# Kernel tuning notes

Measured on AMD Instinct MI355X. Metric: run time of the kernel, lower is better.

The kernel has to match this reference:

```python
import jax, jax.numpy as jnp
import numpy as np

N_NODES = 100000
N_EDGES = 1600000
IN_CH = 64
HID = 64
OUT_CH = 64
N_LAYERS = 4
LN_EPS = 1e-5
GEN_EPS = 1e-7


def setup_inputs() -> dict:
    key = jax.random.key(0)
    ks = jax.random.split(key, 16)
    s = 0.05
    return {
        "x": jax.random.normal(ks[0], (N_NODES, IN_CH), jnp.float32),
        "edge_attr": jax.random.normal(ks[1], (N_EDGES, IN_CH), jnp.float32),
        "edge_index": jax.random.randint(ks[2], (2, N_EDGES), 0, N_NODES, jnp.int32),
        "W_ne": jax.random.normal(ks[3], (IN_CH, HID), jnp.float32) * s,
        "b_ne": jnp.zeros((HID,), jnp.float32),
        "W_ee": jax.random.normal(ks[4], (IN_CH, HID), jnp.float32) * s,
        "b_ee": jnp.zeros((HID,), jnp.float32),
        "W_conv": jax.random.normal(ks[5], (N_LAYERS, HID, HID), jnp.float32) * s,
        "b_conv": jnp.zeros((N_LAYERS, HID), jnp.float32),
        "t": jnp.ones((N_LAYERS,), jnp.float32),
        "gamma": jnp.ones((N_LAYERS, HID), jnp.float32),
        "beta": jnp.zeros((N_LAYERS, HID), jnp.float32),
        "W_lin": jax.random.normal(ks[6], (HID, OUT_CH), jnp.float32) * s,
        "b_lin": jnp.zeros((OUT_CH,), jnp.float32),
    }


def _layer_norm(x, g, b):
    mu = jnp.mean(x, axis=-1, keepdims=True)
    var = jnp.mean(jnp.square(x - mu), axis=-1, keepdims=True)
    return (x - mu) * jax.lax.rsqrt(var + LN_EPS) * g + b


def _gen_conv(h, e, src, dst, W, b, t):
    # GENConv: msg = relu(x_j + edge_attr) + eps; per-dst channel-wise softmax
    # with temperature t; mlp (single Linear) applied to (aggr + x).
    msg = jnp.maximum(h[src] + e, 0.0) + GEN_EPS        # [E, D]
    w = msg * t
    m = jax.ops.segment_max(w, dst, num_segments=N_NODES)  # [N, D]
    ex = jnp.exp(w - m[dst])
    denom = jax.ops.segment_sum(ex, dst, num_segments=N_NODES)
    alpha = ex / (denom[dst] + 1e-16)
    aggr = jax.ops.segment_sum(alpha * msg, dst, num_segments=N_NODES)
    return (aggr + h) @ W + b


def reference(x, edge_attr, edge_index, W_ne, b_ne, W_ee, b_ee,
              W_conv, b_conv, t, gamma, beta, W_lin, b_lin):
    src, dst = edge_index[0], edge_index[1]
    h = x @ W_ne + b_ne              # node_encoder
    e = edge_attr @ W_ee + b_ee      # edge_encoder
    # layers[0].conv applied directly
    h = _gen_conv(h, e, src, dst, W_conv[0], b_conv[0], t[0])
    # remaining layers: pre-norm -> relu -> (dropout=identity, eval) -> conv + residual
    for i in range(1, N_LAYERS):
        z = jnp.maximum(_layer_norm(h, gamma[i], beta[i]), 0.0)
        h = _gen_conv(z, e, src, dst, W_conv[i], b_conv[i], t[i]) + h
    z = jnp.maximum(_layer_norm(h, gamma[0], beta[0]), 0.0)
    return z @ W_lin + b_lin
```

## Files before the change

### kernel.cpp

```cpp
#include <hip/hip_runtime.h>
#include <math.h>

#define NN 100000
#define NE 1600000
#define NB ((NN + 255) / 256)

typedef short bf16x8 __attribute__((ext_vector_type(8)));
typedef unsigned short u16x8 __attribute__((ext_vector_type(8)));
typedef float f32x4 __attribute__((ext_vector_type(4)));
typedef unsigned int u32x4 __attribute__((ext_vector_type(4)));

#define EQ_SCALE 0.025196850393700787f
#define EQ_INV   39.6875f

__device__ __forceinline__ short f2bf(float f) {
    union { float f; unsigned u; } x; x.f = f;
    unsigned r = x.u + 0x7fffu + ((x.u >> 16) & 1u);
    return (short)(r >> 16);
}
__device__ __forceinline__ float bf2f(unsigned short s) {
    union { unsigned u; float f; } x; x.u = ((unsigned)s) << 16;
    return x.f;
}
__device__ __forceinline__ signed char f2q8(float f) {
    float q = rintf(f * EQ_INV);
    q = fminf(127.f, fmaxf(-127.f, q));
    return (signed char)(int)q;
}
__device__ __forceinline__ float q82f(signed char c) {
    return (float)(int)c * EQ_SCALE;
}

__global__ void hist_kernel(const int* __restrict__ dst, int* __restrict__ deg) {
    int i = blockIdx.x * 256 + threadIdx.x;
    if (i < NE) atomicAdd(&deg[dst[i]], 1);
}

__global__ __launch_bounds__(256) void bsum_kernel(const int* __restrict__ deg,
                                                   int* __restrict__ blockSums) {
    __shared__ int sm[256];
    int tid = threadIdx.x, i = blockIdx.x * 256 + tid;
    sm[tid] = (i < NN) ? deg[i] : 0;
    __syncthreads();
    for (int off = 128; off > 0; off >>= 1) {
        if (tid < off) sm[tid] += sm[tid + off];
        __syncthreads();
    }
    if (tid == 0) blockSums[blockIdx.x] = sm[0];
}

__global__ __launch_bounds__(512) void stop_kernel(const int* __restrict__ blockSums,
                                                   int* __restrict__ blockOff) {
    __shared__ int sm[512];
    int tid = threadIdx.x;
    int v = (tid < NB) ? blockSums[tid] : 0;
    sm[tid] = v;
    __syncthreads();
    for (int off = 1; off < 512; off <<= 1) {
        int t = (tid >= off) ? sm[tid - off] : 0;
        __syncthreads();
        sm[tid] += t;
        __syncthreads();
    }
    if (tid < NB) blockOff[tid] = sm[tid] - v;
}

__global__ __launch_bounds__(256) void sfinal_kernel(const int* __restrict__ deg,
                                                     const int* __restrict__ blockOff,
                                                     int* __restrict__ rowStart,
                                                     int* __restrict__ cursor) {
    __shared__ int sm[256];
    int tid = threadIdx.x, i = blockIdx.x * 256 + tid;
    int d = (i < NN) ? deg[i] : 0;
    sm[tid] = d;
    __syncthreads();
    for (int off = 1; off < 256; off <<= 1) {
        int t = (tid >= off) ? sm[tid - off] : 0;
        __syncthreads();
        sm[tid] += t;
        __syncthreads();
    }
    int rs = blockOff[blockIdx.x] + sm[tid] - d;
    if (i < NN) { rowStart[i] = rs; cursor[i] = rs; }
    if (blockIdx.x == 0 && tid == 0) rowStart[NN] = NE;
}

__global__ void scatter_kernel(const int* __restrict__ src, const int* __restrict__ dst,
                               int* __restrict__ cursor, int* __restrict__ ePos,
                               int* __restrict__ srcPerm) {
    int i = blockIdx.x * 256 + threadIdx.x;
    if (i < NE) {
        int d = dst[i];
        int pos = atomicAdd(&cursor[d], 1);
        ePos[i] = pos;
        srcPerm[pos] = src[i];
    }
}

__global__ void prep_weights_kernel(const float* __restrict__ W_ne, const float* __restrict__ W_ee,
                                    const float* __restrict__ W_conv, const float* __restrict__ W_lin,
                                    unsigned short* __restrict__ WT) {
    int id = blockIdx.x * 256 + threadIdx.x;
    if (id >= 7 * 4096) return;
    int mat = id >> 12, idx = id & 4095;
    int n = idx >> 6, k = idx & 63;
    const float* W;
    if (mat == 0) W = W_ne;
    else if (mat == 1) W = W_ee;
    else if (mat <= 5) W = W_conv + (mat - 2) * 4096;
    else W = W_lin;
    WT[id] = (unsigned short)f2bf(W[k * 64 + n]);
}

__global__ __launch_bounds__(256) void gemm64_kernel(
    const void* __restrict__ Av, int aBf16, const unsigned short* __restrict__ WT,
    const float* __restrict__ bias, const float* __restrict__ R,
    const int* __restrict__ scatterPos,
    const float* __restrict__ gLN, const float* __restrict__ bLN,
    unsigned short* __restrict__ zbfOut, void* __restrict__ out, int q8Out, int M)
{
    __shared__ unsigned short tl[4][16][72];
    const int wv   = threadIdx.x >> 6;
    const int lane = threadIdx.x & 63;
    const int m16  = lane & 15;
    const int quad = lane >> 4;
    const int rowBase = blockIdx.x * 64 + wv * 16;

    int r = rowBase + m16;
    long rs = (r < M) ? r : (M - 1);

    bf16x8 afrag[2];
    if (aBf16) {
        const unsigned short* arow = (const unsigned short*)Av + rs * 64;
        #pragma unroll
        for (int s = 0; s < 2; ++s)
            afrag[s] = *(const bf16x8*)(arow + s * 32 + quad * 8);
    } else {
        const float* arow = (const float*)Av + rs * 64;
        #pragma unroll
        for (int s = 0; s < 2; ++s) {
            const float* p = arow + s * 32 + quad * 8;
            #pragma unroll
            for (int j = 0; j < 8; ++j) afrag[s][j] = f2bf(p[j]);
        }
    }

    bf16x8 wfrag[2][4];
    #pragma unroll
    for (int s = 0; s < 2; ++s)
        #pragma unroll
        for (int nt = 0; nt < 4; ++nt)
            wfrag[s][nt] = *(const bf16x8*)(WT + (nt * 16 + m16) * 64 + s * 32 + quad * 8);

    f32x4 acc[4];
    #pragma unroll
    for (int nt = 0; nt < 4; ++nt) acc[nt] = (f32x4){0.f, 0.f, 0.f, 0.f};

    #pragma unroll
    for (int s = 0; s < 2; ++s)
        #pragma unroll
        for (int nt = 0; nt < 4; ++nt)
            acc[nt] = __builtin_amdgcn_mfma_f32_16x16x32_bf16(afrag[s], wfrag[s][nt], acc[nt], 0, 0, 0);

    if (q8Out) {
        signed char* tl8 = (signed char*)tl;
        #pragma unroll
        for (int reg = 0; reg < 4; ++reg)
            #pragma unroll
            for (int nt = 0; nt < 4; ++nt)
                tl8[wv * 1280 + (quad * 4 + reg) * 80 + nt * 16 + m16] =
                    f2q8(acc[nt][reg] + bias[nt * 16 + m16]);
        __syncthreads();
        int r16 = lane >> 2, seg = lane & 3;
        int ro = rowBase + r16;
        if (ro < M) {
            long pos = scatterPos ? (long)scatterPos[ro] : (long)ro;
            u32x4 a = *(const u32x4*)&tl8[wv * 1280 + r16 * 80 + seg * 16];
            *(u32x4*)((signed char*)out + pos * 64 + seg * 16) = a;
        }
        return;
    }

    const int rbase = rowBase + quad * 4;
    #pragma unroll
    for (int reg = 0; reg < 4; ++reg) {
        int ro = rbase + reg;
        if (ro >= M) continue;
        float v[4];
        #pragma unroll
        for (int nt = 0; nt < 4; ++nt) {
            int col = nt * 16 + m16;
            v[nt] = acc[nt][reg] + bias[col];
            if (R) v[nt] += R[(long)ro * 64 + col];
            ((float*)out)[(long)ro * 64 + col] = v[nt];
        }
        if (gLN) {
            float s = v[0] + v[1] + v[2] + v[3];
            #pragma unroll
            for (int off = 1; off < 16; off <<= 1) s += __shfl_xor(s, off);
            float mu = s * (1.f / 64.f);
            float q = 0.f;
            #pragma unroll
            for (int nt = 0; nt < 4; ++nt) { float d = v[nt] - mu; q += d * d; }
            #pragma unroll
            for (int off = 1; off < 16; off <<= 1) q += __shfl_xor(q, off);
            float rstd = rsqrtf(q * (1.f / 64.f) + 1e-5f);
            #pragma unroll
            for (int nt = 0; nt < 4; ++nt) {
                int col = nt * 16 + m16;
                float zv = (v[nt] - mu) * rstd * gLN[col] + bLN[col];
                zbfOut[(long)ro * 64 + col] = (unsigned short)f2bf(fmaxf(zv, 0.f));
            }
        } else if (zbfOut) {
            #pragma unroll
            for (int nt = 0; nt < 4; ++nt) {
                int col = nt * 16 + m16;
                zbfOut[(long)ro * 64 + col] = (unsigned short)f2bf(v[nt]);
            }
        }
    }
}

__global__ __launch_bounds__(256) void agg_kernel(
    const unsigned short* __restrict__ zbf, const signed char* __restrict__ eperm,
    const int* __restrict__ srcPerm, const int* __restrict__ rowStart,
    const float* __restrict__ tArr, int layer, unsigned short* __restrict__ rowbuf)
{
    const int wv = threadIdx.x >> 6, lane = threadIdx.x & 63;
    const int v = blockIdx.x * 4 + wv;
    if (v >= NN) return;
    const float tval = tArr[layer];
    const int s = rowStart[v], e = rowStart[v + 1];

    float selfv = bf2f(zbf[(long)v * 64 + lane]);

    float l = 0.f, ac = 0.f;
    int sp[8];
    if (s < e) {
        #pragma unroll
        for (int k = 0; k < 8; ++k) {
            int jj = s + k; jj = (jj < e) ? jj : (e - 1);
            sp[k] = srcPerm[jj];
        }
    }
    for (int j0 = s; j0 < e; j0 += 8) {
        float zv[8], ev[8];
        #pragma unroll
        for (int k = 0; k < 8; ++k) {
            int jj = j0 + k; jj = (jj < e) ? jj : (e - 1);
            zv[k] = bf2f(zbf[(long)sp[k] * 64 + lane]);
            ev[k] = q82f(eperm[(long)jj * 64 + lane]);
        }
        int spn[8];
        int j1 = j0 + 8;
        if (j1 < e) {
            #pragma unroll
            for (int k = 0; k < 8; ++k) {
                int jj = j1 + k; jj = (jj < e) ? jj : (e - 1);
                spn[k] = srcPerm[jj];
            }
        } else {
            #pragma unroll
            for (int k = 0; k < 8; ++k) spn[k] = sp[k];
        }
        #pragma unroll
        for (int k = 0; k < 8; ++k) {
            if (j0 + k < e) {
                float msg = fmaxf(zv[k] + ev[k], 0.f) + 1e-7f;
                float ex = __expf(msg * tval);
                l += ex;
                ac = fmaf(ex, msg, ac);
            }
        }
        #pragma unroll
        for (int k = 0; k < 8; ++k) sp[k] = spn[k];
    }
    float aggr = ac / (l + 1e-16f);
    rowbuf[(long)v * 64 + lane] = (unsigned short)f2bf(aggr + selfv);
}

extern "C" void kernel_launch(void* const* d_in, const int* in_sizes, int n_in,
                              void* d_out, int out_size, void* d_ws, size_t ws_size,
                              hipStream_t stream) {
    const float* x         = (const float*)d_in[0];
    const float* edge_attr = (const float*)d_in[1];
    const int*   ei        = (const int*)d_in[2];
    const float* W_ne      = (const float*)d_in[3];
    const float* b_ne      = (const float*)d_in[4];
    const float* W_ee      = (const float*)d_in[5];
    const float* b_ee      = (const float*)d_in[6];
    const float* W_conv    = (const float*)d_in[7];
    const float* b_conv    = (const float*)d_in[8];
    const float* t         = (const float*)d_in[9];
    const float* gamma     = (const float*)d_in[10];
    const float* beta      = (const float*)d_in[11];
    const float* W_lin     = (const float*)d_in[12];
    const float* b_lin     = (const float*)d_in[13];

    char* ws = (char*)d_ws;
    float*          h        = (float*)(ws + 0);
    unsigned short* zbf      = (unsigned short*)(ws + 25600000);
    unsigned short* rowbuf   = (unsigned short*)(ws + 51200000);
    signed char*    eperm    = (signed char*)(ws + 64000000);
    int*            ePos     = (int*)(ws + 268800000);
    int*            srcPerm  = (int*)(ws + 275200000);
    int*            deg      = (int*)(ws + 281600000);
    int*            rowStart = (int*)(ws + 282000000);
    int*            cursor   = (int*)(ws + 282400064);
    unsigned short* WT       = (unsigned short*)(ws + 282800064);
    int*            blockSums= (int*)(ws + 282857408);
    int*            blockOff = (int*)(ws + 282859456);

    const int* src = ei;
    const int* dst = ei + NE;

    hipMemsetAsync(deg, 0, NN * sizeof(int), stream);
    hist_kernel<<<(NE + 255) / 256, 256, 0, stream>>>(dst, deg);
    bsum_kernel<<<NB, 256, 0, stream>>>(deg, blockSums);
    stop_kernel<<<1, 512, 0, stream>>>(blockSums, blockOff);
    sfinal_kernel<<<NB, 256, 0, stream>>>(deg, blockOff, rowStart, cursor);
    scatter_kernel<<<(NE + 255) / 256, 256, 0, stream>>>(src, dst, cursor, ePos, srcPerm);
    prep_weights_kernel<<<(7 * 4096 + 255) / 256, 256, 0, stream>>>(W_ne, W_ee, W_conv, W_lin, WT);

    const int gN = (NN + 63) / 64;
    gemm64_kernel<<<gN, 256, 0, stream>>>(x, 0, WT + 0 * 4096, b_ne, nullptr, nullptr,
                                          nullptr, nullptr, zbf, h, 0, NN);
    gemm64_kernel<<<NE / 64, 256, 0, stream>>>(edge_attr, 0, WT + 1 * 4096, b_ee, nullptr, ePos,
                                               nullptr, nullptr, nullptr, eperm, 1, NE);

    agg_kernel<<<NN / 4, 256, 0, stream>>>(zbf, eperm, srcPerm, rowStart, t, 0, rowbuf);
    gemm64_kernel<<<gN, 256, 0, stream>>>(rowbuf, 1, WT + 2 * 4096, b_conv + 0 * 64, nullptr, nullptr,
                                          gamma + 1 * 64, beta + 1 * 64, zbf, h, 0, NN);
    for (int i = 1; i < 4; ++i) {
        int g = (i < 3) ? (i + 1) : 0;
        agg_kernel<<<NN / 4, 256, 0, stream>>>(zbf, eperm, srcPerm, rowStart, t, i, rowbuf);
        gemm64_kernel<<<gN, 256, 0, stream>>>(rowbuf, 1, WT + (2 + i) * 4096, b_conv + i * 64, h, nullptr,
                                              gamma + g * 64, beta + g * 64, zbf, h, 0, NN);
    }
    gemm64_kernel<<<gN, 256, 0, stream>>>(zbf, 1, WT + 6 * 4096, b_lin, nullptr, nullptr,
                                          nullptr, nullptr, nullptr, (float*)d_out, 0, NN);
}
```

Measured before the change: 1.229 ms.

## Fuse aggregation with per-layer GEMM and merge preprocessing kernels

Merges the per-layer aggregation kernel and the following 64x64 GEMM+LayerNorm into one layer kernel: each wave aggregates 16 destination rows into LDS and then runs MFMA on them directly, which removes the rowbuf round trip through global memory and one launch per layer. The histogram, weight transpose and node-encoder GEMM are combined into a single launch. Edge scatter is fused into the edge-encoder GEMM, dropping the ePos array. The cost is less parallelism in aggregation (one wave walks 16 nodes in sequence instead of one node per wave), ping-pong z buffers, and a serialised degree-skewed loop inside the GEMM blocks.

```diff
diff --git a/kernel.cpp b/kernel.cpp
--- a/kernel.cpp
+++ b/kernel.cpp
@@ -4,6 +4,9 @@
 #define NN 100000
 #define NE 1600000
 #define NB ((NN + 255) / 256)
+#define GN ((NN + 63) / 64)
+#define HIST_BLKS (NE / 256)
+#define PREP_BLKS (7 * 4096 / 256)
 
 typedef short bf16x8 __attribute__((ext_vector_type(8)));
 typedef unsigned short u16x8 __attribute__((ext_vector_type(8)));
@@ -29,11 +32,6 @@
 }
 __device__ __forceinline__ float q82f(signed char c) {
     return (float)(int)c * EQ_SCALE;
-}
-
-__global__ void hist_kernel(const int* __restrict__ dst, int* __restrict__ deg) {
-    int i = blockIdx.x * 256 + threadIdx.x;
-    if (i < NE) atomicAdd(&deg[dst[i]], 1);
 }
 
 __global__ __launch_bounds__(256) void bsum_kernel(const int* __restrict__ deg,
@@ -85,198 +83,305 @@
     if (blockIdx.x == 0 && tid == 0) rowStart[NN] = NE;
 }
 
-__global__ void scatter_kernel(const int* __restrict__ src, const int* __restrict__ dst,
-                               int* __restrict__ cursor, int* __restrict__ ePos,
-                               int* __restrict__ srcPerm) {
-    int i = blockIdx.x * 256 + threadIdx.x;
-    if (i < NE) {
+__global__ __launch_bounds__(256) void pre_kernel(
+    const int* __restrict__ dst, int* __restrict__ deg,
+    const float* __restrict__ W_ne, const float* __restrict__ W_ee,
+    const float* __restrict__ W_conv, const float* __restrict__ W_lin,
+    unsigned short* __restrict__ WT,
+    const float* __restrict__ x, const float* __restrict__ b_ne,
+    float* __restrict__ h, unsigned short* __restrict__ zbf0)
+{
+    int b = blockIdx.x;
+    if (b < HIST_BLKS) {
+        int i = b * 256 + threadIdx.x;
+        atomicAdd(&deg[dst[i]], 1);
+        return;
+    }
+    b -= HIST_BLKS;
+    if (b < PREP_BLKS) {
+        int id = b * 256 + threadIdx.x;
+        int mat = id >> 12, idx = id & 4095;
+        int n = idx >> 6, k = idx & 63;
+        const float* W;
+        if (mat == 0) W = W_ne;
+        else if (mat == 1) W = W_ee;
+        else if (mat <= 5) W = W_conv + (mat - 2) * 4096;
+        else W = W_lin;
+        WT[id] = (unsigned short)f2bf(W[k * 64 + n]);
+        return;
+    }
+    b -= PREP_BLKS;
+    const int wv = threadIdx.x >> 6, lane = threadIdx.x & 63;
+    const int m16 = lane & 15, quad = lane >> 4;
+    const int rowBase = b * 64 + wv * 16;
+    int r = rowBase + m16;
+    long rs = (r < NN) ? r : (NN - 1);
+
+    bf16x8 afrag[2];
+    #pragma unroll
+    for (int s = 0; s < 2; ++s) {
+        const float* p = x + rs * 64 + s * 32 + quad * 8;
+        #pragma unroll
+        for (int j = 0; j < 8; ++j) afrag[s][j] = f2bf(p[j]);
+    }
+    bf16x8 wfrag[2][4];
+    #pragma unroll
+    for (int s = 0; s < 2; ++s)
+        #pragma unroll
+        for (int nt = 0; nt < 4; ++nt)
+            #pragma unroll
+            for (int j = 0; j < 8; ++j)
+                wfrag[s][nt][j] = f2bf(W_ne[(s * 32 + quad * 8 + j) * 64 + nt * 16 + m16]);
+
+    f32x4 acc[4];
+    #pragma unroll
+    for (int nt = 0; nt < 4; ++nt) acc[nt] = (f32x4){0.f, 0.f, 0.f, 0.f};
+    #pragma unroll
+    for (int s = 0; s < 2; ++s)
+        #pragma unroll
+        for (int nt = 0; nt < 4; ++nt)
+            acc[nt] = __builtin_amdgcn_mfma_f32_16x16x32_bf16(afrag[s], wfrag[s][nt], acc[nt], 0, 0, 0);
+
+    const int rbase = rowBase + quad * 4;
+    #pragma unroll
+    for (int reg = 0; reg < 4; ++reg) {
+        int ro = rbase + reg;
+        if (ro >= NN) continue;
+        #pragma unroll
+        for (int nt = 0; nt < 4; ++nt) {
+            int col = nt * 16 + m16;
+            float v = acc[nt][reg] + b_ne[col];
+            h[(long)ro * 64 + col] = v;
+            zbf0[(long)ro * 64 + col] = (unsigned short)f2bf(v);
+        }
+    }
+}
+
+__global__ __launch_bounds__(256) void edge_kernel(
+    const float* __restrict__ edge_attr, const int* __restrict__ src, const int* __restrict__ dst,
+    int* __restrict__ cursor, int* __restrict__ srcPerm,
+    const unsigned short* __restrict__ WT_ee, const float* __restrict__ b_ee,
+    signed char* __restrict__ eperm)
+{
+    __shared__ int posLds[64];
+    __shared__ signed char tl8[4 * 1280];
+    const int wv = threadIdx.x >> 6, lane = threadIdx.x & 63;
+    const int m16 = lane & 15, quad = lane >> 4;
+    const int rowBase = blockIdx.x * 64;
+
+    if (threadIdx.x < 64) {
+        int i = rowBase + threadIdx.x;
         int d = dst[i];
         int pos = atomicAdd(&cursor[d], 1);
-        ePos[i] = pos;
         srcPerm[pos] = src[i];
-    }
-}
-
-__global__ void prep_weights_kernel(const float* __restrict__ W_ne, const float* __restrict__ W_ee,
-                                    const float* __restrict__ W_conv, const float* __restrict__ W_lin,
-                                    unsigned short* __restrict__ WT) {
-    int id = blockIdx.x * 256 + threadIdx.x;
-    if (id >= 7 * 4096) return;
-    int mat = id >> 12, idx = id & 4095;
-    int n = idx >> 6, k = idx & 63;
-    const float* W;
-    if (mat == 0) W = W_ne;
-    else if (mat == 1) W = W_ee;
-    else if (mat <= 5) W = W_conv + (mat - 2) * 4096;
-    else W = W_lin;
-    WT[id] = (unsigned short)f2bf(W[k * 64 + n]);
-}
-
-__global__ __launch_bounds__(256) void gemm64_kernel(
-    const void* __restrict__ Av, int aBf16, const unsigned short* __restrict__ WT,
-    const float* __restrict__ bias, const float* __restrict__ R,
-    const int* __restrict__ scatterPos,
+        posLds[threadIdx.x] = pos;
+    }
+
+    long rs = rowBase + wv * 16 + m16;
+    bf16x8 afrag[2];
+    #pragma unroll
+    for (int s = 0; s < 2; ++s) {
+        const float* p = edge_attr + rs * 64 + s * 32 + quad * 8;
+        #pragma unroll
+        for (int j = 0; j < 8; ++j) afrag[s][j] = f2bf(p[j]);
+    }
+    bf16x8 wfrag[2][4];
+    #pragma unroll
+    for (int s = 0; s < 2; ++s)
+        #pragma unroll
+        for (int nt = 0; nt < 4; ++nt)
+            wfrag[s][nt] = *(const bf16x8*)(WT_ee + (nt * 16 + m16) * 64 + s * 32 + quad * 8);
+
+    f32x4 acc[4];
+    #pragma unroll
+    for (int nt = 0; nt < 4; ++nt) acc[nt] = (f32x4){0.f, 0.f, 0.f, 0.f};
+    #pragma unroll
+    for (int s = 0; s < 2; ++s)
+        #pragma unroll
+        for (int nt = 0; nt < 4; ++nt)
+            acc[nt] = __builtin_amdgcn_mfma_f32_16x16x32_bf16(afrag[s], wfrag[s][nt], acc[nt], 0, 0, 0);
+
+    signed char* t8 = tl8 + wv * 1280;
+    #pragma unroll
+    for (int reg = 0; reg < 4; ++reg)
+        #pragma unroll
+        for (int nt = 0; nt < 4; ++nt)
+            t8[(quad * 4 + reg) * 80 + nt * 16 + m16] =
+                f2q8(acc[nt][reg] + b_ee[nt * 16 + m16]);
+    __syncthreads();
+    int r16 = lane >> 2, seg = lane & 3;
+    long pos = posLds[wv * 16 + r16];
+    u32x4 a = *(const u32x4*)&tl8[wv * 1280 + r16 * 80 + seg * 16];
+    *(u32x4*)(eperm + pos * 64 + seg * 16) = a;
+}
+
+__global__ __launch_bounds__(256) void layer_kernel(
+    const unsigned short* __restrict__ zin, const signed char* __restrict__ eperm,
+    const int* __restrict__ srcPerm, const int* __restrict__ rowStart,
+    const float* __restrict__ tArr, int layer,
+    const unsigned short* __restrict__ WT_l, const float* __restrict__ bias,
+    const float* __restrict__ R, float* __restrict__ hout,
     const float* __restrict__ gLN, const float* __restrict__ bLN,
-    unsigned short* __restrict__ zbfOut, void* __restrict__ out, int q8Out, int M)
+    unsigned short* __restrict__ zout)
 {
     __shared__ unsigned short tl[4][16][72];
-    const int wv   = threadIdx.x >> 6;
-    const int lane = threadIdx.x & 63;
-    const int m16  = lane & 15;
-    const int quad = lane >> 4;
+    const int wv = threadIdx.x >> 6, lane = threadIdx.x & 63;
+    const int m16 = lane & 15, quad = lane >> 4;
     const int rowBase = blockIdx.x * 64 + wv * 16;
-
-    int r = rowBase + m16;
-    long rs = (r < M) ? r : (M - 1);
+    const float tval = tArr[layer];
+
+    int rsv = 0;
+    if (lane < 17) {
+        int idx = rowBase + lane;
+        rsv = rowStart[idx <= NN ? idx : NN];
+    }
+
+    for (int n = 0; n < 16; ++n) {
+        int v = rowBase + n;
+        float res = 0.f;
+        if (v < NN) {
+            int s = __shfl(rsv, n), e = __shfl(rsv, n + 1);
+            float l = 0.f, ac = 0.f;
+            int sp[8];
+            if (s < e) {
+                #pragma unroll
+                for (int k = 0; k < 8; ++k) {
+                    int jj = s + k; jj = (jj < e) ? jj : (e - 1);
+                    sp[k] = srcPerm[jj];
+                }
+            }
+            for (int j0 = s; j0 < e; j0 += 8) {
+                float zvv[8], evv[8];
+                #pragma unroll
+                for (int k = 0; k < 8; ++k) {
+                    int jj = j0 + k; jj = (jj < e) ? jj : (e - 1);
+                    zvv[k] = bf2f(zin[(long)sp[k] * 64 + lane]);
+                    evv[k] = q82f(eperm[(long)jj * 64 + lane]);
+                }
+                int spn[8];
+                int j1 = j0 + 8;
+                if (j1 < e) {
+                    #pragma unroll
+                    for (int k = 0; k < 8; ++k) {
+                        int jj = j1 + k; jj = (jj < e) ? jj : (e - 1);
+                        spn[k] = srcPerm[jj];
+                    }
+                } else {
+                    #pragma unroll
+                    for (int k = 0; k < 8; ++k) spn[k] = sp[k];
+                }
+                #pragma unroll
+                for (int k = 0; k < 8; ++k) {
+                    if (j0 + k < e) {
+                        float msg = fmaxf(zvv[k] + evv[k], 0.f) + 1e-7f;
+                        float ex = __expf(msg * tval);
+                        l += ex;
+                        ac = fmaf(ex, msg, ac);
+                    }
+                }
+                #pragma unroll
+                for (int k = 0; k < 8; ++k) sp[k] = spn[k];
+            }
+            float aggr = ac / (l + 1e-16f);
+            res = aggr + bf2f(zin[(long)v * 64 + lane]);
+        }
+        tl[wv][n][lane] = (unsigned short)f2bf(res);
+    }
+    __syncthreads();
 
     bf16x8 afrag[2];
-    if (aBf16) {
-        const unsigned short* arow = (const unsigned short*)Av + rs * 64;
-        #pragma unroll
-        for (int s = 0; s < 2; ++s)
-            afrag[s] = *(const bf16x8*)(arow + s * 32 + quad * 8);
-    } else {
-        const float* arow = (const float*)Av + rs * 64;
-        #pragma unroll
-        for (int s = 0; s < 2; ++s) {
-            const float* p = arow + s * 32 + quad * 8;
-            #pragma unroll
-            for (int j = 0; j < 8; ++j) afrag[s][j] = f2bf(p[j]);
-        }
-    }
-
+    #pragma unroll
+    for (int s = 0; s < 2; ++s)
+        afrag[s] = *(const bf16x8*)&tl[wv][m16][s * 32 + quad * 8];
     bf16x8 wfrag[2][4];
     #pragma unroll
     for (int s = 0; s < 2; ++s)
         #pragma unroll
         for (int nt = 0; nt < 4; ++nt)
-            wfrag[s][nt] = *(const bf16x8*)(WT + (nt * 16 + m16) * 64 + s * 32 + quad * 8);
+            wfrag[s][nt] = *(const bf16x8*)(WT_l + (nt * 16 + m16) * 64 + s * 32 + quad * 8);
 
     f32x4 acc[4];
     #pragma unroll
     for (int nt = 0; nt < 4; ++nt) acc[nt] = (f32x4){0.f, 0.f, 0.f, 0.f};
-
     #pragma unroll
     for (int s = 0; s < 2; ++s)
         #pragma unroll
         for (int nt = 0; nt < 4; ++nt)
             acc[nt] = __builtin_amdgcn_mfma_f32_16x16x32_bf16(afrag[s], wfrag[s][nt], acc[nt], 0, 0, 0);
 
-    if (q8Out) {
-        signed char* tl8 = (signed char*)tl;
-        #pragma unroll
-        for (int reg = 0; reg < 4; ++reg)
-            #pragma unroll
-            for (int nt = 0; nt < 4; ++nt)
-                tl8[wv * 1280 + (quad * 4 + reg) * 80 + nt * 16 + m16] =
-                    f2q8(acc[nt][reg] + bias[nt * 16 + m16]);
-        __syncthreads();
-        int r16 = lane >> 2, seg = lane & 3;
-        int ro = rowBase + r16;
-        if (ro < M) {
-            long pos = scatterPos ? (long)scatterPos[ro] : (long)ro;
-            u32x4 a = *(const u32x4*)&tl8[wv * 1280 + r16 * 80 + seg * 16];
-            *(u32x4*)((signed char*)out + pos * 64 + seg * 16) = a;
-        }
-        return;
-    }
-
-    const int rbase = rowBase + quad * 4;
+    const int rbase = blockIdx.x * 64 + wv * 16 + quad * 4;
     #pragma unroll
     for (int reg = 0; reg < 4; ++reg) {
         int ro = rbase + reg;
-        if (ro >= M) continue;
+        if (ro >= NN) continue;
         float v[4];
         #pragma unroll
         for (int nt = 0; nt < 4; ++nt) {
             int col = nt * 16 + m16;
             v[nt] = acc[nt][reg] + bias[col];
             if (R) v[nt] += R[(long)ro * 64 + col];
-            ((float*)out)[(long)ro * 64 + col] = v[nt];
+            if (hout) hout[(long)ro * 64 + col] = v[nt];
         }
-        if (gLN) {
-            float s = v[0] + v[1] + v[2] + v[3];
-            #pragma unroll
-            for (int off = 1; off < 16; off <<= 1) s += __shfl_xor(s, off);
-            float mu = s * (1.f / 64.f);
-            float q = 0.f;
-            #pragma unroll
-            for (int nt = 0; nt < 4; ++nt) { float d = v[nt] - mu; q += d * d; }
-            #pragma unroll
-            for (int off = 1; off < 16; off <<= 1) q += __shfl_xor(q, off);
-            float rstd = rsqrtf(q * (1.f / 64.f) + 1e-5f);
-            #pragma unroll
-            for (int nt = 0; nt < 4; ++nt) {
-                int col = nt * 16 + m16;
-                float zv = (v[nt] - mu) * rstd * gLN[col] + bLN[col];
-                zbfOut[(long)ro * 64 + col] = (unsigned short)f2bf(fmaxf(zv, 0.f));
-            }
-        } else if (zbfOut) {
-            #pragma unroll
-            for (int nt = 0; nt < 4; ++nt) {
-                int col = nt * 16 + m16;
-                zbfOut[(long)ro * 64 + col] = (unsigned short)f2bf(v[nt]);
-            }
+        float s = v[0] + v[1] + v[2] + v[3];
+        #pragma unroll
+        for (int off = 1; off < 16; off <<= 1) s += __shfl_xor(s, off);
+        float mu = s * (1.f / 64.f);
+        float q = 0.f;
+        #pragma unroll
+        for (int nt = 0; nt < 4; ++nt) { float d = v[nt] - mu; q += d * d; }
+        #pragma unroll
+        for (int off = 1; off < 16; off <<= 1) q += __shfl_xor(q, off);
+        float rstd = rsqrtf(q * (1.f / 64.f) + 1e-5f);
+        #pragma unroll
+        for (int nt = 0; nt < 4; ++nt) {
+            int col = nt * 16 + m16;
+            float zv = (v[nt] - mu) * rstd * gLN[col] + bLN[col];
+            zout[(long)ro * 64 + col] = (unsigned short)f2bf(fmaxf(zv, 0.f));
         }
     }
 }
 
-__global__ __launch_bounds__(256) void agg_kernel(
-    const unsigned short* __restrict__ zbf, const signed char* __restrict__ eperm,
-    const int* __restrict__ srcPerm, const int* __restrict__ rowStart,
-    const float* __restrict__ tArr, int layer, unsigned short* __restrict__ rowbuf)
+__global__ __launch_bounds__(256) void final_kernel(
+    const unsigned short* __restrict__ zin, const unsigned short* __restrict__ WT_lin,
+    const float* __restrict__ b_lin, float* __restrict__ out)
 {
     const int wv = threadIdx.x >> 6, lane = threadIdx.x & 63;
-    const int v = blockIdx.x * 4 + wv;
-    if (v >= NN) return;
-    const float tval = tArr[layer];
-    const int s = rowStart[v], e = rowStart[v + 1];
-
-    float selfv = bf2f(zbf[(long)v * 64 + lane]);
-
-    float l = 0.f, ac = 0.f;
-    int sp[8];
-    if (s < e) {
-        #pragma unroll
-        for (int k = 0; k < 8; ++k) {
-            int jj = s + k; jj = (jj < e) ? jj : (e - 1);
-            sp[k] = srcPerm[jj];
+    const int m16 = lane & 15, quad = lane >> 4;
+    const int rowBase = blockIdx.x * 64 + wv * 16;
+    int r = rowBase + m16;
+    long rs = (r < NN) ? r : (NN - 1);
+
+    bf16x8 afrag[2];
+    #pragma unroll
+    for (int s = 0; s < 2; ++s)
+        afrag[s] = *(const bf16x8*)((const unsigned short*)zin + rs * 64 + s * 32 + quad * 8);
+    bf16x8 wfrag[2][4];
+    #pragma unroll
+    for (int s = 0; s < 2; ++s)
+        #pragma unroll
+        for (int nt = 0; nt < 4; ++nt)
+            wfrag[s][nt] = *(const bf16x8*)(WT_lin + (nt * 16 + m16) * 64 + s * 32 + quad * 8);
+
+    f32x4 acc[4];
+    #pragma unroll
+    for (int nt = 0; nt < 4; ++nt) acc[nt] = (f32x4){0.f, 0.f, 0.f, 0.f};
+    #pragma unroll
+    for (int s = 0; s < 2; ++s)
+        #pragma unroll
+        for (int nt = 0; nt < 4; ++nt)
+            acc[nt] = __builtin_amdgcn_mfma_f32_16x16x32_bf16(afrag[s], wfrag[s][nt], acc[nt], 0, 0, 0);
+
+    const int rbase = rowBase + quad * 4;
+    #pragma unroll
+    for (int reg = 0; reg < 4; ++reg) {
+        int ro = rbase + reg;
+        if (ro >= NN) continue;
+        #pragma unroll
+        for (int nt = 0; nt < 4; ++nt) {
+            int col = nt * 16 + m16;
+            out[(long)ro * 64 + col] = acc[nt][reg] + b_lin[col];
         }
     }
-    for (int j0 = s; j0 < e; j0 += 8) {
-        float zv[8], ev[8];
-        #pragma unroll
-        for (int k = 0; k < 8; ++k) {
-            int jj = j0 + k; jj = (jj < e) ? jj : (e - 1);
-            zv[k] = bf2f(zbf[(long)sp[k] * 64 + lane]);
-            ev[k] = q82f(eperm[(long)jj * 64 + lane]);
-        }
-        int spn[8];
-        int j1 = j0 + 8;
-        if (j1 < e) {
-            #pragma unroll
-            for (int k = 0; k < 8; ++k) {
-                int jj = j1 + k; jj = (jj < e) ? jj : (e - 1);
-                spn[k] = srcPerm[jj];
-            }
-        } else {
-            #pragma unroll
-            for (int k = 0; k < 8; ++k) spn[k] = sp[k];
-        }
-        #pragma unroll
-        for (int k = 0; k < 8; ++k) {
-            if (j0 + k < e) {
-                float msg = fmaxf(zv[k] + ev[k], 0.f) + 1e-7f;
-                float ex = __expf(msg * tval);
-                l += ex;
-                ac = fmaf(ex, msg, ac);
-            }
-        }
-        #pragma unroll
-        for (int k = 0; k < 8; ++k) sp[k] = spn[k];
-    }
-    float aggr = ac / (l + 1e-16f);
-    rowbuf[(long)v * 64 + lane] = (unsigned short)f2bf(aggr + selfv);
 }
 
 extern "C" void kernel_launch(void* const* d_in, const int* in_sizes, int n_in,
@@ -299,10 +404,9 @@
 
     char* ws = (char*)d_ws;
     float*          h        = (float*)(ws + 0);
-    unsigned short* zbf      = (unsigned short*)(ws + 25600000);
-    unsigned short* rowbuf   = (unsigned short*)(ws + 51200000);
+    unsigned short* zbf0     = (unsigned short*)(ws + 25600000);
+    unsigned short* zbf1     = (unsigned short*)(ws + 38400000);
     signed char*    eperm    = (signed char*)(ws + 64000000);
-    int*            ePos     = (int*)(ws + 268800000);
     int*            srcPerm  = (int*)(ws + 275200000);
     int*            deg      = (int*)(ws + 281600000);
     int*            rowStart = (int*)(ws + 282000000);
@@ -315,28 +419,25 @@
     const int* dst = ei + NE;
 
     hipMemsetAsync(deg, 0, NN * sizeof(int), stream);
-    hist_kernel<<<(NE + 255) / 256, 256, 0, stream>>>(dst, deg);
+    pre_kernel<<<HIST_BLKS + PREP_BLKS + GN, 256, 0, stream>>>(
+        dst, deg, W_ne, W_ee, W_conv, W_lin, WT, x, b_ne, h, zbf0);
     bsum_kernel<<<NB, 256, 0, stream>>>(deg, blockSums);
     stop_kernel<<<1, 512, 0, stream>>>(blockSums, blockOff);
     sfinal_kernel<<<NB, 256, 0, stream>>>(deg, blockOff, rowStart, cursor);
-    scatter_kernel<<<(NE + 255) / 256, 256, 0, stream>>>(src, dst, cursor, ePos, srcPerm);
-    prep_weights_kernel<<<(7 * 4096 + 255) / 256, 256, 0, stream>>>(W_ne, W_ee, W_conv, W_lin, WT);
-
-    const int gN = (NN + 63) / 64;
-    gemm64_kernel<<<gN, 256, 0, stream>>>(x, 0, WT + 0 * 4096, b_ne, nullptr, nullptr,
-                                          nullptr, nullptr, zbf, h, 0, NN);
-    gemm64_kernel<<<NE / 64, 256, 0, stream>>>(edge_attr, 0, WT + 1 * 4096, b_ee, nullptr, ePos,
-                                               nullptr, nullptr, nullptr, eperm, 1, NE);
-
-    agg_kernel<<<NN / 4, 256, 0, stream>>>(zbf, eperm, srcPerm, rowStart, t, 0, rowbuf);
-    gemm64_kernel<<<gN, 256, 0, stream>>>(rowbuf, 1, WT + 2 * 4096, b_conv + 0 * 64, nullptr, nullptr,
-                                          gamma + 1 * 64, beta + 1 * 64, zbf, h, 0, NN);
-    for (int i = 1; i < 4; ++i) {
+    edge_kernel<<<NE / 64, 256, 0, stream>>>(edge_attr, src, dst, cursor, srcPerm,
+                                             WT + 1 * 4096, b_ee, eperm);
+
+    unsigned short* zi = zbf0;
+    unsigned short* zo = zbf1;
+    for (int i = 0; i < 4; ++i) {
         int g = (i < 3) ? (i + 1) : 0;
-        agg_kernel<<<NN / 4, 256, 0, stream>>>(zbf, eperm, srcPerm, rowStart, t, i, rowbuf);
-        gemm64_kernel<<<gN, 256, 0, stream>>>(rowbuf, 1, WT + (2 + i) * 4096, b_conv + i * 64, h, nullptr,
-                                              gamma + g * 64, beta + g * 64, zbf, h, 0, NN);
-    }
-    gemm64_kernel<<<gN, 256, 0, stream>>>(zbf, 1, WT + 6 * 4096, b_lin, nullptr, nullptr,
-                                          nullptr, nullptr, nullptr, (float*)d_out, 0, NN);
-}
+        layer_kernel<<<GN, 256, 0, stream>>>(
+            zi, eperm, srcPerm, rowStart, t, i,
+            WT + (2 + i) * 4096, b_conv + i * 64,
+            (i > 0) ? h : nullptr,
+            (i < 3) ? h : nullptr,
+            gamma + g * 64, beta + g * 64, zo);
+        unsigned short* tmp = zi; zi = zo; zo = tmp;
+    }
+    final_kernel<<<GN, 256, 0, stream>>>(zi, WT + 6 * 4096, b_lin, (float*)d_out);
+}
```

Measured after the change: 1.265 ms. 2.9% more time.
